# Kernel tuning notes

Measured on AMD Instinct MI355X. Metric: run time of the kernel, lower is better.

Reference implementation:

```python
import jax, jax.numpy as jnp
import numpy as np

BSZ, P, D, C = 16, 4096, 256, 512


def setup_inputs() -> dict:
    key = jax.random.key(0)
    k1, k2 = jax.random.split(key)
    x = jax.random.normal(k1, (BSZ, P, D), dtype=jnp.float32)
    kernels = jax.random.normal(k2, (C, D), dtype=jnp.float32) * 0.001
    return {"x": x, "kernels": kernels}


def reference(x, kernels):
    bsz, Pn, d = x.shape
    # (bsz, P, C) projection scores, ReLU'd
    scores = jax.nn.relu(jnp.einsum('bpd,cd->bpc', x, kernels))
    # per-channel argmax over positions -> (bsz, C)
    idx = jnp.argmax(scores, axis=1)
    # scatter_add each kernel row into its winning position
    b_idx = jnp.arange(bsz)[:, None]  # (bsz, 1) broadcast against (bsz, C)
    src = jnp.broadcast_to(kernels, (bsz,) + kernels.shape)  # (bsz, C, d)
    out = jnp.zeros((bsz, Pn, d), dtype=x.dtype).at[b_idx, idx].add(src)
    return out
```

## Files before the change

### kernel.cpp

```cpp
#include <hip/hip_runtime.h>
#include <cstddef>
#include <cstdint>

#define BSZ 16
#define PN  4096
#define DD  256
#define CC  512
#define TP  128
#define TC  64
#define NPT (PN / TP)
#define NCT (CC / TC)
#define NKC 8

typedef short bf16x8 __attribute__((ext_vector_type(8)));
typedef float f32x4  __attribute__((ext_vector_type(4)));

struct Top2 { float v1, v2; int i1, i2; };

__device__ __forceinline__ void t2_insert(Top2& t, float v, int i) {
  if (v > t.v1 || (v == t.v1 && i < t.i1)) {
    t.v2 = t.v1; t.i2 = t.i1; t.v1 = v; t.i1 = i;
  } else if (v > t.v2 || (v == t.v2 && i < t.i2)) {
    t.v2 = v; t.i2 = i;
  }
}

__device__ __forceinline__ void split4(float4 v, uint2& hp, uint2& lp) {
  uint32_t u0 = __float_as_uint(v.x), u1 = __float_as_uint(v.y),
           u2 = __float_as_uint(v.z), u3 = __float_as_uint(v.w);
  float l0 = v.x - __uint_as_float(u0 & 0xffff0000u);
  float l1 = v.y - __uint_as_float(u1 & 0xffff0000u);
  float l2 = v.z - __uint_as_float(u2 & 0xffff0000u);
  float l3 = v.w - __uint_as_float(u3 & 0xffff0000u);
  hp.x = __builtin_amdgcn_perm(u1, u0, 0x07060302u);
  hp.y = __builtin_amdgcn_perm(u3, u2, 0x07060302u);
  lp.x = __builtin_amdgcn_perm(__float_as_uint(l1), __float_as_uint(l0), 0x07060302u);
  lp.y = __builtin_amdgcn_perm(__float_as_uint(l3), __float_as_uint(l2), 0x07060302u);
}

__global__ __launch_bounds__(256) void convert_k_kernel(
    const float* __restrict__ kern, uint32_t* __restrict__ ks) {
  const int kc = blockIdx.x, ct = blockIdx.y;
  const size_t chunk = ((size_t)ct * NKC + kc) * 4096;
  int s  = threadIdx.x + blockIdx.z * 256;
  int fp = s >> 6, kg = (s >> 4) & 3, lr = s & 15;
  int r  = fp * 16 + lr, k0 = kg * 8;
  const float* src = kern + ((size_t)ct * 128 + r) * DD + kc * 32 + k0;
  float4 v0 = *(const float4*)src, v1 = *(const float4*)(src + 4);
  uint2 h0, l0, h1, l1; split4(v0, h0, l0); split4(v1, h1, l1);
  *(uint4*)&ks[chunk + (size_t)s * 4]        = make_uint4(h0.x, h0.y, h1.x, h1.y);
  *(uint4*)&ks[chunk + 2048 + (size_t)s * 4] = make_uint4(l0.x, l0.y, l1.x, l1.y);
}

__global__ __launch_bounds__(256, 3) void score_kernel(
    const float* __restrict__ x, const uint32_t* __restrict__ ks,
    float2* __restrict__ pv2, uint32_t* __restrict__ pix) {

  __shared__ __align__(16) float4 scratch[16 * TC];

  const int d  = blockIdx.x;
  const int L  = (d & 7) * 512 + (d >> 3);
  const int ct = L & 7;
  const int pt = (L >> 3) & 31;
  const int b  = L >> 8;

  const int tid = threadIdx.x;
  const int lane = tid & 63, w = tid >> 6;
  const int lr = lane & 15, kg = lane >> 4;

  const char* bbase = (const char*)ks + (size_t)(ct >> 1) * NKC * 16384
                    + (ct & 1) * 4096 + lane * 16;

  const char* xbase = (const char*)(x + ((size_t)b * PN + (size_t)pt * TP) * DD);
  const char* ap[2][2];
#pragma unroll
  for (int fp = 0; fp < 2; fp++)
#pragma unroll
    for (int h = 0; h < 2; h++)
      ap[fp][h] = xbase + (size_t)(w * 32 + fp * 16 + lr) * (DD * 4) + kg * 32 + h * 16;

  f32x4 acc[2][4];
#pragma unroll
  for (int i = 0; i < 2; i++)
#pragma unroll
    for (int j = 0; j < 4; j++) acc[i][j] = (f32x4)0.f;

#pragma unroll
  for (int kc = 0; kc < NKC; kc++) {
    bf16x8 Bh[4], Bl[4];
#pragma unroll
    for (int fc = 0; fc < 4; fc++) {
      Bh[fc] = *(const bf16x8*)(bbase + kc * 16384 +        fc * 1024);
      Bl[fc] = *(const bf16x8*)(bbase + kc * 16384 + 8192 + fc * 1024);
    }
    bf16x8 Ah[2], Al[2];
#pragma unroll
    for (int fp = 0; fp < 2; fp++) {
      float4 v0 = *(const float4*)(ap[fp][0] + kc * 128);
      float4 v1 = *(const float4*)(ap[fp][1] + kc * 128);
      uint2 h0, l0, h1, l1; split4(v0, h0, l0); split4(v1, h1, l1);
      uint4 hh = make_uint4(h0.x, h0.y, h1.x, h1.y);
      uint4 ll = make_uint4(l0.x, l0.y, l1.x, l1.y);
      Ah[fp] = *(bf16x8*)&hh;
      Al[fp] = *(bf16x8*)&ll;
    }
#pragma unroll
    for (int fc = 0; fc < 4; fc++) {
#pragma unroll
      for (int fp = 0; fp < 2; fp++) {
        acc[fp][fc] = __builtin_amdgcn_mfma_f32_16x16x32_bf16(Ah[fp], Bh[fc], acc[fp][fc], 0, 0, 0);
        acc[fp][fc] = __builtin_amdgcn_mfma_f32_16x16x32_bf16(Ah[fp], Bl[fc], acc[fp][fc], 0, 0, 0);
        acc[fp][fc] = __builtin_amdgcn_mfma_f32_16x16x32_bf16(Al[fp], Bh[fc], acc[fp][fc], 0, 0, 0);
      }
    }
  }

  const int slot = w * 4 + kg;
#pragma unroll
  for (int fc = 0; fc < 4; fc++) {
    Top2 t; t.v1 = -1.f; t.v2 = -1.f; t.i1 = 0x7fffffff; t.i2 = 0x7fffffff;
#pragma unroll
    for (int fp = 0; fp < 2; fp++)
#pragma unroll
      for (int r = 0; r < 4; r++) {
        float v = acc[fp][fc][r]; v = v > 0.f ? v : 0.f;
        t2_insert(t, v, w * 32 + fp * 16 + kg * 4 + r);
      }
    scratch[slot * TC + fc * 16 + lr] =
        make_float4(t.v1, __int_as_float(t.i1), t.v2, __int_as_float(t.i2));
  }
  __syncthreads();

  if (tid < TC) {
    Top2 t; t.v1 = -1.f; t.v2 = -1.f; t.i1 = 0x7fffffff; t.i2 = 0x7fffffff;
#pragma unroll
    for (int s = 0; s < 16; s++) {
      float4 e = scratch[s * TC + tid];
      t2_insert(t, e.x, __float_as_int(e.y));
      t2_insert(t, e.z, __float_as_int(e.w));
    }
    int c = ct * TC + tid;
    size_t o = ((size_t)b * CC + c) * NPT + pt;
    uint32_t p1 = (uint32_t)(pt * TP + t.i1);
    uint32_t p2 = (uint32_t)(pt * TP + t.i2);
    pv2[o] = make_float2(t.v1, t.v2);
    pix[o] = (p1 << 16) | (p2 & 0xffffu);
  }
}

__global__ __launch_bounds__(256) void reduce_winner_kernel(
    const float2* __restrict__ pv2, const uint32_t* __restrict__ pix,
    const float* __restrict__ x, const float* __restrict__ kern,
    int* __restrict__ winner) {
  const int b = blockIdx.y;
  const int c = blockIdx.x * 4 + (threadIdx.x >> 6);
  const int l = threadIdx.x & 63;

  Top2 t; t.v1 = -1.f; t.v2 = -1.f; t.i1 = 0x7fffffff; t.i2 = 0x7fffffff;
  if (l < NPT) {
    size_t o = ((size_t)b * CC + c) * NPT + l;
    float2 v = pv2[o]; uint32_t ii = pix[o];
    t.v1 = v.x; t.v2 = v.y; t.i1 = (int)(ii >> 16); t.i2 = (int)(ii & 0xffffu);
  }
#pragma unroll
  for (int m = 1; m < 64; m <<= 1) {
    float uv1 = __shfl_xor(t.v1, m, 64);
    int   ui1 = __shfl_xor(t.i1, m, 64);
    float uv2 = __shfl_xor(t.v2, m, 64);
    int   ui2 = __shfl_xor(t.i2, m, 64);
    t2_insert(t, uv1, ui1);
    t2_insert(t, uv2, ui2);
  }

  int win = t.i1;
  if (t.v1 - t.v2 <= 1e-4f * t.v1 + 1e-5f) {
    const float4* x1 = (const float4*)(x + ((size_t)b * PN + t.i1) * DD);
    const float4* x2 = (const float4*)(x + ((size_t)b * PN + t.i2) * DD);
    const float4* kc = (const float4*)(kern + (size_t)c * DD);
    float4 a1 = x1[l], a2 = x2[l], k4 = kc[l];
    float s1 = a1.x * k4.x + a1.y * k4.y + a1.z * k4.z + a1.w * k4.w;
    float s2 = a2.x * k4.x + a2.y * k4.y + a2.z * k4.z + a2.w * k4.w;
#pragma unroll
    for (int m = 1; m < 64; m <<= 1) {
      s1 += __shfl_xor(s1, m, 64);
      s2 += __shfl_xor(s2, m, 64);
    }
    s1 = fmaxf(s1, 0.f); s2 = fmaxf(s2, 0.f);
    if (s2 > s1 || (s2 == s1 && t.i2 < t.i1)) win = t.i2;
  }
  if (l == 0) winner[(size_t)b * CC + c] = win;
}

__global__ __launch_bounds__(256) void write_out_kernel(
    const int* __restrict__ winner, const float* __restrict__ kern,
    float4* __restrict__ out) {
  __shared__ __align__(16) int wrow[CC];
  const int b = blockIdx.y;
  const int tid = threadIdx.x, lane = tid & 63, w = tid >> 6;
  const int p = blockIdx.x * 4 + w;

  *(int2*)&wrow[tid * 2] = *(const int2*)&winner[(size_t)b * CC + tid * 2];
  __syncthreads();

  int4 w0 = *(const int4*)&wrow[lane * 8];
  int4 w1 = *(const int4*)&wrow[lane * 8 + 4];
  int wv[8] = {w0.x, w0.y, w0.z, w0.w, w1.x, w1.y, w1.z, w1.w};

  float4 acc = make_float4(0.f, 0.f, 0.f, 0.f);
#pragma unroll
  for (int j = 0; j < 8; j++) {
    unsigned long long m = __ballot(wv[j] == p);
    while (m) {
      int bit = __ffsll((long long)m) - 1; m &= m - 1;
      int c = bit * 8 + j;
      float4 kv = ((const float4*)(kern + (size_t)c * DD))[lane];
      acc.x += kv.x; acc.y += kv.y; acc.z += kv.z; acc.w += kv.w;
    }
  }
  out[((size_t)b * PN + p) * 64 + lane] = acc;
}

extern "C" void kernel_launch(void* const* d_in, const int* in_sizes, int n_in,
                              void* d_out, int out_size, void* d_ws, size_t ws_size,
                              hipStream_t stream) {
  const float* x    = (const float*)d_in[0];
  const float* kern = (const float*)d_in[1];
  float* out = (float*)d_out;

  char* ws = (char*)d_ws;
  float2*   pv2 = (float2*)ws;
  uint32_t* pix = (uint32_t*)(ws + (size_t)BSZ * CC * NPT * sizeof(float2));
  uint32_t* ks  = (uint32_t*)(ws + 3u * 1024 * 1024);
  int*      win = (int*)(ws + 3u * 1024 * 1024 + 512u * 1024);

  convert_k_kernel<<<dim3(NKC, CC / 128, 2), 256, 0, stream>>>(kern, ks);

  score_kernel<<<dim3(NCT * NPT * BSZ), 256, 0, stream>>>(x, ks, pv2, pix);

  reduce_winner_kernel<<<dim3(CC / 4, BSZ), 256, 0, stream>>>(pv2, pix, x, kern, win);

  write_out_kernel<<<dim3(PN / 4, BSZ), 256, 0, stream>>>(win, kern, (float4*)out);
}
```

Before: 208.8 us.

## Double-buffer global loads in score kernel and regroup MFMAs with priority

```diff
diff --git a/kernel.cpp b/kernel.cpp
--- a/kernel.cpp
+++ b/kernel.cpp
@@ -14,6 +14,9 @@
 
 typedef short bf16x8 __attribute__((ext_vector_type(8)));
 typedef float f32x4  __attribute__((ext_vector_type(4)));
+
+#define MEMFENCE() __asm__ __volatile__("" ::: "memory")
+#define WAITCNT_VM0 0x1F70
 
 struct Top2 { float v1, v2; int i1, i2; };
 
@@ -79,6 +82,28 @@
     for (int h = 0; h < 2; h++)
       ap[fp][h] = xbase + (size_t)(w * 32 + fp * 16 + lr) * (DD * 4) + kg * 32 + h * 16;
 
+  float4 abuf[2][2][2];
+  bf16x8 Bh[2][4], Bl[2][4];
+
+  auto load = [&](int kc) {
+    const int p = kc & 1;
+#pragma unroll
+    for (int fc = 0; fc < 4; fc++) {
+      Bh[p][fc] = *(const bf16x8*)(bbase + kc * 16384 +        fc * 1024);
+      Bl[p][fc] = *(const bf16x8*)(bbase + kc * 16384 + 8192 + fc * 1024);
+    }
+#pragma unroll
+    for (int fp = 0; fp < 2; fp++)
+#pragma unroll
+      for (int h = 0; h < 2; h++)
+        abuf[p][fp][h] = *(const float4*)(ap[fp][h] + kc * 128);
+  };
+
+  load(0);
+  MEMFENCE();
+  __builtin_amdgcn_s_waitcnt(WAITCNT_VM0);
+  __builtin_amdgcn_sched_barrier(0);
+
   f32x4 acc[2][4];
 #pragma unroll
   for (int i = 0; i < 2; i++)
@@ -87,31 +112,43 @@
 
 #pragma unroll
   for (int kc = 0; kc < NKC; kc++) {
-    bf16x8 Bh[4], Bl[4];
-#pragma unroll
-    for (int fc = 0; fc < 4; fc++) {
-      Bh[fc] = *(const bf16x8*)(bbase + kc * 16384 +        fc * 1024);
-      Bl[fc] = *(const bf16x8*)(bbase + kc * 16384 + 8192 + fc * 1024);
-    }
+    const int p = kc & 1;
+    if (kc + 1 < NKC) load(kc + 1);
+    __builtin_amdgcn_sched_barrier(0);
+
     bf16x8 Ah[2], Al[2];
 #pragma unroll
     for (int fp = 0; fp < 2; fp++) {
-      float4 v0 = *(const float4*)(ap[fp][0] + kc * 128);
-      float4 v1 = *(const float4*)(ap[fp][1] + kc * 128);
-      uint2 h0, l0, h1, l1; split4(v0, h0, l0); split4(v1, h1, l1);
+      uint2 h0, l0, h1, l1;
+      split4(abuf[p][fp][0], h0, l0);
+      split4(abuf[p][fp][1], h1, l1);
       uint4 hh = make_uint4(h0.x, h0.y, h1.x, h1.y);
       uint4 ll = make_uint4(l0.x, l0.y, l1.x, l1.y);
       Ah[fp] = *(bf16x8*)&hh;
       Al[fp] = *(bf16x8*)&ll;
     }
-#pragma unroll
-    for (int fc = 0; fc < 4; fc++) {
-#pragma unroll
-      for (int fp = 0; fp < 2; fp++) {
-        acc[fp][fc] = __builtin_amdgcn_mfma_f32_16x16x32_bf16(Ah[fp], Bh[fc], acc[fp][fc], 0, 0, 0);
-        acc[fp][fc] = __builtin_amdgcn_mfma_f32_16x16x32_bf16(Ah[fp], Bl[fc], acc[fp][fc], 0, 0, 0);
-        acc[fp][fc] = __builtin_amdgcn_mfma_f32_16x16x32_bf16(Al[fp], Bh[fc], acc[fp][fc], 0, 0, 0);
-      }
+    __builtin_amdgcn_s_setprio(1);
+#pragma unroll
+    for (int fc = 0; fc < 4; fc++)
+#pragma unroll
+      for (int fp = 0; fp < 2; fp++)
+        acc[fp][fc] = __builtin_amdgcn_mfma_f32_16x16x32_bf16(Ah[fp], Bh[p][fc], acc[fp][fc], 0, 0, 0);
+#pragma unroll
+    for (int fc = 0; fc < 4; fc++)
+#pragma unroll
+      for (int fp = 0; fp < 2; fp++)
+        acc[fp][fc] = __builtin_amdgcn_mfma_f32_16x16x32_bf16(Ah[fp], Bl[p][fc], acc[fp][fc], 0, 0, 0);
+#pragma unroll
+    for (int fc = 0; fc < 4; fc++)
+#pragma unroll
+      for (int fp = 0; fp < 2; fp++)
+        acc[fp][fc] = __builtin_amdgcn_mfma_f32_16x16x32_bf16(Al[fp], Bh[p][fc], acc[fp][fc], 0, 0, 0);
+    __builtin_amdgcn_s_setprio(0);
+    __builtin_amdgcn_sched_barrier(0);
+    if (kc + 1 < NKC) {
+      MEMFENCE();
+      __builtin_amdgcn_s_waitcnt(WAITCNT_VM0);
+      __builtin_amdgcn_sched_barrier(0);
     }
   }
 
@@ -229,7 +266,7 @@
 
   char* ws = (char*)d_ws;
   float2*   pv2 = (float2*)ws;
-  uint32_t* pix = (uint32_t*)(ws + (size_t)BSZ * CC * NPT * sizeof(float2));
+  uint32_t* pix = (uint32_t*)(ws + 2u * 1024 * 1024);
   uint32_t* ks  = (uint32_t*)(ws + 3u * 1024 * 1024);
   int*      win = (int*)(ws + 3u * 1024 * 1024 + 512u * 1024);
 
```

Result: no change. 206.9 us (-0.9%).
